# Kernel tuning notes

Hardware: AMD Instinct MI355X
Metric: run time of the kernel (lower is better)

The kernel has to match this reference:

```python
import jax, jax.numpy as jnp
import numpy as np

# Hyperparameters (match init_kwargs)
NOSHF_S = 64
NOSHF_R = 64
NOSHF_THETA = 64
LOWER_S, UPPER_S = -3.0, 3.0
LOWER_R, UPPER_R = -3.0, 3.0
LOWER_THETA, UPPER_THETA = 0.0, float(np.pi)
OETA_S = 8.0
OETA_R = 8.0
OZETA = 8.0
Z_TABLE = np.array([1, 6, 7, 8, 9, 16, 17])  # H C N O F S Cl -> rows 0..6
NCONF, NATOMS = 256, 128


def setup_inputs() -> dict:
    key = jax.random.key(0)
    k1, k2, k3, k4 = jax.random.split(key, 4)
    coefficients = jax.random.normal(k1, (NCONF, NATOMS, 21), dtype=jnp.float32)
    mus = jax.random.normal(k2, (2, 7, 9), dtype=jnp.float32) * 0.1
    sigmas = jax.random.uniform(k3, (2, 7, 9), dtype=jnp.float32, minval=0.5, maxval=1.5)
    # order: s_coeffs_mus, s_coeffs_sigmas, p_norms_mus, p_norms_sigmas
    normalization_library = jnp.stack([mus[0], sigmas[0], mus[1], sigmas[1]], axis=0)
    codes = jax.random.randint(k4, (NCONF, NATOMS), 0, 7)
    species = jnp.asarray(Z_TABLE, dtype=jnp.int64 if jax.config.jax_enable_x64 else jnp.int32)[codes]
    return {"coefficients": coefficients, "normalization_library": normalization_library, "species": species}


def reference(coefficients, normalization_library, species):
    nc, na, _ = coefficients.shape
    # species Z -> table row index
    z = jnp.asarray(Z_TABLE)
    sidx = jnp.argmax(species[..., None] == z, axis=-1)  # (nc, na)

    s_mus, s_sig, p_mus, p_sig = normalization_library
    p_mus = p_mus[:, :4]
    p_sig = p_sig[:, :4]

    # s-type coefficients: normalize then gaussian-shift expand
    s = coefficients[:, :, :9]
    s = (s - s_mus[sidx]) / s_sig[sidx]  # (nc, na, 9)
    shfS = jnp.linspace(LOWER_S, UPPER_S, NOSHF_S, dtype=jnp.float32)
    s_aev = jnp.exp(-OETA_S * (s[..., None] - shfS) ** 2).reshape(nc, na, 9 * NOSHF_S)

    # p-type: orbital matrix (nc, na, 4 AOVs, 3) -> norms, normalize, radial expand
    M = coefficients[:, :, 9:21].reshape(nc, na, 4, 3)
    p_norms = jnp.linalg.norm(M, axis=-1)  # (nc, na, 4)
    p_norms = (p_norms - p_mus[sidx]) / p_sig[sidx]
    shfR = jnp.linspace(LOWER_R, UPPER_R, NOSHF_R, dtype=jnp.float32)
    r_aev = jnp.exp(-OETA_R * (p_norms[..., None] - shfR) ** 2).reshape(nc, na, 4 * NOSHF_R)

    # angles between AOVs (rows normalized by the *normalized* norms, as in source)
    zero_mask = jnp.all(jnp.abs(M) < 1e-12, axis=-1)  # (nc, na, 4)
    Mn = jnp.where(zero_mask[..., None], 0.0, M / p_norms[..., None])
    G = jnp.einsum('bnik,bnjk->bnij', Mn, Mn)  # (nc, na, 4, 4)
    iu, ju = np.triu_indices(4, 1)  # 6 pairs, same row-major order as the loops
    cos_angles = jnp.clip(G[:, :, iu, ju], -0.9999, 0.9999)  # (nc, na, 6)
    angles = jnp.arccos(cos_angles)

    shfT = jnp.linspace(LOWER_THETA, UPPER_THETA, NOSHF_THETA, dtype=jnp.float32)
    ang = (2.0 ** (1.0 - OZETA)) * ((1.0 + jnp.cos(angles[..., None] - shfT)) / 2.0) ** OZETA
    ang_aev = ang.reshape(nc, na, 6 * NOSHF_THETA)

    return jnp.concatenate([s_aev, r_aev, ang_aev], axis=-1)  # (nc, na, 1216)
```

## Files before the change

### kernel.cpp

```cpp
#include <hip/hip_runtime.h>
#include <hip/hip_bf16.h>
#include <math.h>

#define NCONF  256
#define NATOMS 128
#define NATOT  (NCONF * NATOMS)
#define PER_ATOM 1216
#define ABLK   16
#define NBLK   (NATOT / ABLK)

#define SQK      3.3972871196167196f
#define SK_STEP  0.32355115424921137f
#define SK_BASE -10.191861358850159f
#define HS       0.27262693316631437f

__device__ __forceinline__ int species_to_sidx(int z) {
    switch (z) {
        case 1:  return 0;
        case 6:  return 1;
        case 7:  return 2;
        case 8:  return 3;
        case 9:  return 4;
        case 16: return 5;
        default: return 6;
    }
}

__global__ __launch_bounds__(256) void aev_fused_kernel(
    const float* __restrict__ coeff,
    const float* __restrict__ nlib,
    const int*   __restrict__ sp32,
    float* __restrict__ out)
{
    __shared__ float c_sh[ABLK][21];
    __shared__ float pars[ABLK][25];
    __shared__ float Mn_sh[ABLK][4][3];
    __shared__ int   sidx_sh[ABLK];
    __shared__ float ct_sh[64], st_sh[64];

    const int tid = threadIdx.x;
    const int a0  = blockIdx.x * ABLK;

    if (tid < 64) {
        float t = (float)tid * (float)(M_PI / 63.0);
        ct_sh[tid] = __cosf(t);
        st_sh[tid] = __sinf(t);
    }
    #pragma unroll
    for (int i = tid; i < ABLK * 21; i += 256) {
        c_sh[i / 21][i % 21] = coeff[(size_t)a0 * 21 + i];
    }
    if (tid < ABLK) {
        const int is64 = (sp32[1] == 0);
        const int atom = a0 + tid;
        const int z = is64 ? sp32[(size_t)atom * 2] : sp32[atom];
        sidx_sh[tid] = species_to_sidx(z);
    }
    __syncthreads();

    if (tid < 144) {
        int a = tid / 9, k = tid - a * 9;
        int sidx = sidx_sh[a];
        float mu = nlib[0 * 63 + sidx * 9 + k];
        float sg = nlib[1 * 63 + sidx * 9 + k];
        pars[a][k] = SQK * (c_sh[a][k] - mu) / sg;
    } else if (tid < 208) {
        int t = tid - 144;
        int a = t >> 2, i = t & 3;
        float x = c_sh[a][9 + i * 3 + 0];
        float y = c_sh[a][9 + i * 3 + 1];
        float w = c_sh[a][9 + i * 3 + 2];
        float nn  = x * x + y * y + w * w;
        float nrm = sqrtf(nn);
        bool zero = (fabsf(x) < 1e-12f) && (fabsf(y) < 1e-12f) &&
                    (fabsf(w) < 1e-12f);
        int sidx = sidx_sh[a];
        float mu = nlib[2 * 63 + sidx * 9 + i];
        float sg = nlib[3 * 63 + sidx * 9 + i];
        pars[a][9 + i] = SQK * (nrm - mu) / sg;
        float inv = zero ? 0.0f : (1.0f / nrm);
        Mn_sh[a][i][0] = x * inv;
        Mn_sh[a][i][1] = y * inv;
        Mn_sh[a][i][2] = w * inv;
    }
    __syncthreads();

    if (tid < 96) {
        int a = tid / 6, p = tid - a * 6;
        const int iu[6] = {0, 0, 0, 1, 1, 2};
        const int ju[6] = {1, 2, 3, 2, 3, 3};
        int i = iu[p], j = ju[p];
        float d = Mn_sh[a][i][0] * Mn_sh[a][j][0] +
                  Mn_sh[a][i][1] * Mn_sh[a][j][1] +
                  Mn_sh[a][i][2] * Mn_sh[a][j][2];
        d = fminf(fmaxf(d, -0.9999f), 0.9999f);
        float sa = sqrtf(fmaxf(1.0f - d * d, 0.0f));
        pars[a][13 + p] = HS * d;
        pars[a][19 + p] = HS * sa;
    }
    __syncthreads();

    float* po_blk = out + (size_t)a0 * PER_ATOM;

    #pragma unroll
    for (int it = 0; it < 13; ++it) {
        int idx = it * 256 + tid;
        int a   = idx / 208;
        int rq  = idx - a * 208;
        float X = pars[a][rq >> 4];
        float b = fmaf((float)((rq & 15) << 2), SK_STEP, SK_BASE);
        float d0 = X - b;
        float d1 = d0 - SK_STEP;
        float d2 = d1 - SK_STEP;
        float d3 = d2 - SK_STEP;
        float4 v;
        v.x = exp2f(-(d0 * d0));
        v.y = exp2f(-(d1 * d1));
        v.z = exp2f(-(d2 * d2));
        v.w = exp2f(-(d3 * d3));
        *reinterpret_cast<float4*>(po_blk + a * PER_ATOM + rq * 4) = v;
    }

    #pragma unroll
    for (int it = 0; it < 6; ++it) {
        int idx = it * 256 + tid;
        int a   = idx / 96;
        int aq  = idx - a * 96;
        int p   = aq >> 4;
        int j0  = (aq & 15) << 2;
        float Ap = pars[a][13 + p];
        float Bp = pars[a][19 + p];
        float4 ct = *reinterpret_cast<const float4*>(&ct_sh[j0]);
        float4 st = *reinterpret_cast<const float4*>(&st_sh[j0]);
        float u0 = fmaf(Ap, ct.x, fmaf(Bp, st.x, HS));
        float u1 = fmaf(Ap, ct.y, fmaf(Bp, st.y, HS));
        float u2 = fmaf(Ap, ct.z, fmaf(Bp, st.z, HS));
        float u3 = fmaf(Ap, ct.w, fmaf(Bp, st.w, HS));
        float4 v;
        u0 *= u0; u0 *= u0; v.x = u0 * u0;
        u1 *= u1; u1 *= u1; v.y = u1 * u1;
        u2 *= u2; u2 *= u2; v.z = u2 * u2;
        u3 *= u3; u3 *= u3; v.w = u3 * u3;
        *reinterpret_cast<float4*>(po_blk + a * PER_ATOM + 832 + aq * 4) = v;
    }
}

extern "C" void kernel_launch(void* const* d_in, const int* in_sizes, int n_in,
                              void* d_out, int out_size, void* d_ws, size_t ws_size,
                              hipStream_t stream) {
    const float* coeff   = (const float*)d_in[0];
    const float* nlib    = (const float*)d_in[1];
    const int*   sp32    = (const int*)d_in[2];
    float* out           = (float*)d_out;

    aev_fused_kernel<<<dim3(NBLK), dim3(256), 0, stream>>>(
        coeff, nlib, sp32, out);
}
```

Before: 31.84 us.

## Process two atom groups per block with register prefetch of next group's inputs

```diff
diff --git a/kernel.cpp b/kernel.cpp
--- a/kernel.cpp
+++ b/kernel.cpp
@@ -7,7 +7,8 @@
 #define NATOT  (NCONF * NATOMS)
 #define PER_ATOM 1216
 #define ABLK   16
-#define NBLK   (NATOT / ABLK)
+#define GRPS   2
+#define NBLK   (NATOT / (ABLK * GRPS))
 
 #define SQK      3.3972871196167196f
 #define SK_STEP  0.32355115424921137f
@@ -26,7 +27,7 @@
     }
 }
 
-__global__ __launch_bounds__(256) void aev_fused_kernel(
+__global__ __launch_bounds__(256) void aev_persist_kernel(
     const float* __restrict__ coeff,
     const float* __restrict__ nlib,
     const int*   __restrict__ sp32,
@@ -39,7 +40,9 @@
     __shared__ float ct_sh[64], st_sh[64];
 
     const int tid = threadIdx.x;
-    const int a0  = blockIdx.x * ABLK;
+    const int a0  = blockIdx.x * (ABLK * GRPS);
+
+    const int is64 = (sp32[1] == 0);
 
     if (tid < 64) {
         float t = (float)tid * (float)(M_PI / 63.0);
@@ -51,97 +54,123 @@
         c_sh[i / 21][i % 21] = coeff[(size_t)a0 * 21 + i];
     }
     if (tid < ABLK) {
-        const int is64 = (sp32[1] == 0);
         const int atom = a0 + tid;
         const int z = is64 ? sp32[(size_t)atom * 2] : sp32[atom];
         sidx_sh[tid] = species_to_sidx(z);
     }
     __syncthreads();
 
-    if (tid < 144) {
-        int a = tid / 9, k = tid - a * 9;
-        int sidx = sidx_sh[a];
-        float mu = nlib[0 * 63 + sidx * 9 + k];
-        float sg = nlib[1 * 63 + sidx * 9 + k];
-        pars[a][k] = SQK * (c_sh[a][k] - mu) / sg;
-    } else if (tid < 208) {
-        int t = tid - 144;
-        int a = t >> 2, i = t & 3;
-        float x = c_sh[a][9 + i * 3 + 0];
-        float y = c_sh[a][9 + i * 3 + 1];
-        float w = c_sh[a][9 + i * 3 + 2];
-        float nn  = x * x + y * y + w * w;
-        float nrm = sqrtf(nn);
-        bool zero = (fabsf(x) < 1e-12f) && (fabsf(y) < 1e-12f) &&
-                    (fabsf(w) < 1e-12f);
-        int sidx = sidx_sh[a];
-        float mu = nlib[2 * 63 + sidx * 9 + i];
-        float sg = nlib[3 * 63 + sidx * 9 + i];
-        pars[a][9 + i] = SQK * (nrm - mu) / sg;
-        float inv = zero ? 0.0f : (1.0f / nrm);
-        Mn_sh[a][i][0] = x * inv;
-        Mn_sh[a][i][1] = y * inv;
-        Mn_sh[a][i][2] = w * inv;
-    }
-    __syncthreads();
+    #pragma unroll
+    for (int g = 0; g < GRPS; ++g) {
+        if (tid < 144) {
+            int a = tid / 9, k = tid - a * 9;
+            int sidx = sidx_sh[a];
+            float mu = nlib[0 * 63 + sidx * 9 + k];
+            float sg = nlib[1 * 63 + sidx * 9 + k];
+            pars[a][k] = SQK * (c_sh[a][k] - mu) / sg;
+        } else if (tid < 208) {
+            int t = tid - 144;
+            int a = t >> 2, i = t & 3;
+            float x = c_sh[a][9 + i * 3 + 0];
+            float y = c_sh[a][9 + i * 3 + 1];
+            float w = c_sh[a][9 + i * 3 + 2];
+            float nn  = x * x + y * y + w * w;
+            float nrm = sqrtf(nn);
+            bool zero = (fabsf(x) < 1e-12f) && (fabsf(y) < 1e-12f) &&
+                        (fabsf(w) < 1e-12f);
+            int sidx = sidx_sh[a];
+            float mu = nlib[2 * 63 + sidx * 9 + i];
+            float sg = nlib[3 * 63 + sidx * 9 + i];
+            pars[a][9 + i] = SQK * (nrm - mu) / sg;
+            float inv = zero ? 0.0f : (1.0f / nrm);
+            Mn_sh[a][i][0] = x * inv;
+            Mn_sh[a][i][1] = y * inv;
+            Mn_sh[a][i][2] = w * inv;
+        }
+        __syncthreads();
 
-    if (tid < 96) {
-        int a = tid / 6, p = tid - a * 6;
-        const int iu[6] = {0, 0, 0, 1, 1, 2};
-        const int ju[6] = {1, 2, 3, 2, 3, 3};
-        int i = iu[p], j = ju[p];
-        float d = Mn_sh[a][i][0] * Mn_sh[a][j][0] +
-                  Mn_sh[a][i][1] * Mn_sh[a][j][1] +
-                  Mn_sh[a][i][2] * Mn_sh[a][j][2];
-        d = fminf(fmaxf(d, -0.9999f), 0.9999f);
-        float sa = sqrtf(fmaxf(1.0f - d * d, 0.0f));
-        pars[a][13 + p] = HS * d;
-        pars[a][19 + p] = HS * sa;
-    }
-    __syncthreads();
+        if (tid < 96) {
+            int a = tid / 6, p = tid - a * 6;
+            const int iu[6] = {0, 0, 0, 1, 1, 2};
+            const int ju[6] = {1, 2, 3, 2, 3, 3};
+            int i = iu[p], j = ju[p];
+            float d = Mn_sh[a][i][0] * Mn_sh[a][j][0] +
+                      Mn_sh[a][i][1] * Mn_sh[a][j][1] +
+                      Mn_sh[a][i][2] * Mn_sh[a][j][2];
+            d = fminf(fmaxf(d, -0.9999f), 0.9999f);
+            float sa = sqrtf(fmaxf(1.0f - d * d, 0.0f));
+            pars[a][13 + p] = HS * d;
+            pars[a][19 + p] = HS * sa;
+        }
+        __syncthreads();
 
-    float* po_blk = out + (size_t)a0 * PER_ATOM;
+        float pf0 = 0.0f, pf1 = 0.0f;
+        int   sidx_n = 0;
+        if (g + 1 < GRPS) {
+            const float* cn = coeff + ((size_t)a0 + (g + 1) * ABLK) * 21;
+            pf0 = cn[tid];
+            if (tid < ABLK * 21 - 256) pf1 = cn[256 + tid];
+            if (tid < ABLK) {
+                const int atom = a0 + (g + 1) * ABLK + tid;
+                const int z = is64 ? sp32[(size_t)atom * 2] : sp32[atom];
+                sidx_n = species_to_sidx(z);
+            }
+        }
 
-    #pragma unroll
-    for (int it = 0; it < 13; ++it) {
-        int idx = it * 256 + tid;
-        int a   = idx / 208;
-        int rq  = idx - a * 208;
-        float X = pars[a][rq >> 4];
-        float b = fmaf((float)((rq & 15) << 2), SK_STEP, SK_BASE);
-        float d0 = X - b;
-        float d1 = d0 - SK_STEP;
-        float d2 = d1 - SK_STEP;
-        float d3 = d2 - SK_STEP;
-        float4 v;
-        v.x = exp2f(-(d0 * d0));
-        v.y = exp2f(-(d1 * d1));
-        v.z = exp2f(-(d2 * d2));
-        v.w = exp2f(-(d3 * d3));
-        *reinterpret_cast<float4*>(po_blk + a * PER_ATOM + rq * 4) = v;
-    }
+        float* po_blk = out + (size_t)(a0 + g * ABLK) * PER_ATOM;
 
-    #pragma unroll
-    for (int it = 0; it < 6; ++it) {
-        int idx = it * 256 + tid;
-        int a   = idx / 96;
-        int aq  = idx - a * 96;
-        int p   = aq >> 4;
-        int j0  = (aq & 15) << 2;
-        float Ap = pars[a][13 + p];
-        float Bp = pars[a][19 + p];
-        float4 ct = *reinterpret_cast<const float4*>(&ct_sh[j0]);
-        float4 st = *reinterpret_cast<const float4*>(&st_sh[j0]);
-        float u0 = fmaf(Ap, ct.x, fmaf(Bp, st.x, HS));
-        float u1 = fmaf(Ap, ct.y, fmaf(Bp, st.y, HS));
-        float u2 = fmaf(Ap, ct.z, fmaf(Bp, st.z, HS));
-        float u3 = fmaf(Ap, ct.w, fmaf(Bp, st.w, HS));
-        float4 v;
-        u0 *= u0; u0 *= u0; v.x = u0 * u0;
-        u1 *= u1; u1 *= u1; v.y = u1 * u1;
-        u2 *= u2; u2 *= u2; v.z = u2 * u2;
-        u3 *= u3; u3 *= u3; v.w = u3 * u3;
-        *reinterpret_cast<float4*>(po_blk + a * PER_ATOM + 832 + aq * 4) = v;
+        #pragma unroll
+        for (int it = 0; it < 13; ++it) {
+            int idx = it * 256 + tid;
+            int a   = idx / 208;
+            int rq  = idx - a * 208;
+            float X = pars[a][rq >> 4];
+            float b = fmaf((float)((rq & 15) << 2), SK_STEP, SK_BASE);
+            float d0 = X - b;
+            float d1 = d0 - SK_STEP;
+            float d2 = d1 - SK_STEP;
+            float d3 = d2 - SK_STEP;
+            float4 v;
+            v.x = exp2f(-(d0 * d0));
+            v.y = exp2f(-(d1 * d1));
+            v.z = exp2f(-(d2 * d2));
+            v.w = exp2f(-(d3 * d3));
+            *reinterpret_cast<float4*>(po_blk + a * PER_ATOM + rq * 4) = v;
+        }
+
+        #pragma unroll
+        for (int it = 0; it < 6; ++it) {
+            int idx = it * 256 + tid;
+            int a   = idx / 96;
+            int aq  = idx - a * 96;
+            int p   = aq >> 4;
+            int j0  = (aq & 15) << 2;
+            float Ap = pars[a][13 + p];
+            float Bp = pars[a][19 + p];
+            float4 ct = *reinterpret_cast<const float4*>(&ct_sh[j0]);
+            float4 st = *reinterpret_cast<const float4*>(&st_sh[j0]);
+            float u0 = fmaf(Ap, ct.x, fmaf(Bp, st.x, HS));
+            float u1 = fmaf(Ap, ct.y, fmaf(Bp, st.y, HS));
+            float u2 = fmaf(Ap, ct.z, fmaf(Bp, st.z, HS));
+            float u3 = fmaf(Ap, ct.w, fmaf(Bp, st.w, HS));
+            float4 v;
+            u0 *= u0; u0 *= u0; v.x = u0 * u0;
+            u1 *= u1; u1 *= u1; v.y = u1 * u1;
+            u2 *= u2; u2 *= u2; v.z = u2 * u2;
+            u3 *= u3; u3 *= u3; v.w = u3 * u3;
+            *reinterpret_cast<float4*>(po_blk + a * PER_ATOM + 832 + aq * 4) = v;
+        }
+
+        if (g + 1 < GRPS) {
+            __syncthreads();
+            c_sh[tid / 21][tid % 21] = pf0;
+            if (tid < ABLK * 21 - 256) {
+                int i2 = 256 + tid;
+                c_sh[i2 / 21][i2 % 21] = pf1;
+            }
+            if (tid < ABLK) sidx_sh[tid] = sidx_n;
+            __syncthreads();
+        }
     }
 }
 
@@ -153,6 +182,6 @@
     const int*   sp32    = (const int*)d_in[2];
     float* out           = (float*)d_out;
 
-    aev_fused_kernel<<<dim3(NBLK), dim3(256), 0, stream>>>(
+    aev_persist_kernel<<<dim3(NBLK), dim3(256), 0, stream>>>(
         coeff, nlib, sp32, out);
 }
```

Measured after the change: 32.04 us. About the same (+0.6%).
